# Kernel tuning notes

Measured on AMD Instinct MI355X. Metric: run time of the kernel, lower is better.

The kernel has to match this reference:

```python
import jax, jax.numpy as jnp
import numpy as np
from jax import lax


def setup_inputs() -> dict:
    key = jax.random.key(0)
    k1, k2 = jax.random.split(key)
    B, H, W, Cin, Cout, kh, kw = 16, 128, 128, 128, 128, 3, 3
    X = jax.random.normal(k1, (B, H, W, Cin), dtype=jnp.float32)
    kernel = jax.random.normal(k2, (B, kh, kw, Cin, Cout), dtype=jnp.float32) * 0.05
    return {"X": X, "kernel": kernel}


def _conv_one(x, k):
    # x: [H, W, Cin]; k: [kh, kw, Cin, Cout] -> [H', W', Cout]
    out = lax.conv_general_dilated(
        x[None],  # [1, H, W, Cin]
        k,
        window_strides=(1, 1),
        padding='VALID',
        dimension_numbers=('NHWC', 'HWIO', 'NHWC'),
    )
    return out[0]


def reference(X, kernel):
    # Per-sample dynamic-filter conv: each batch element convolved with its own
    # [kh, kw, Cin, Cout] filter. Equivalent to the TF depthwise-reshape trick
    # followed by reduce_sum over the input-channel axis.
    return jax.vmap(_conv_one)(X, kernel)  # [B, H', W', Cout]
```

## Files before the change

kernel.cpp:

```cpp
#include <hip/hip_runtime.h>
#include <cstdint>

#define OWD 126
#define MTOT 15876

typedef short bf16x8 __attribute__((ext_vector_type(8)));
typedef float f32x4  __attribute__((ext_vector_type(4)));

#define BT_ELEMS  (16u * 128u * 1152u)
#define XBF_ELEMS (16u * 128u * 128u * 128u)
#define WS_NEEDED ((size_t)(BT_ELEMS + XBF_ELEMS) * 2)

__device__ __forceinline__ uint16_t f2bf(float f) {
    union { float f; uint32_t u; } v;
    v.f = f;
    uint32_t u = v.u;
    return (uint16_t)((u + 0x7FFFu + ((u >> 16) & 1u)) >> 16);
}

__device__ __forceinline__ uint32_t pk2(float a, float b) {
    return (uint32_t)f2bf(a) | ((uint32_t)f2bf(b) << 16);
}

__device__ __forceinline__ void gl_lds16(const uint16_t* g, uint16_t* l) {
    __builtin_amdgcn_global_load_lds(
        (const __attribute__((address_space(1))) uint32_t*)g,
        (__attribute__((address_space(3))) uint32_t*)l, 16, 0, 0);
}

__global__ __launch_bounds__(256) void kprep(const float* __restrict__ Kin,
                                             uint16_t* __restrict__ Bt) {
    const int rs = blockIdx.x;
    const int b  = blockIdx.y;
    const int t  = threadIdx.x;
    const int n  = t & 127;
    const int og = t >> 7;

    const float* src = Kin + (((size_t)b * 9 + rs) << 14);
    uint16_t*    dst = Bt + ((size_t)b * 128 + n) * 1152 + rs * 128;

#pragma unroll
    for (int o = 0; o < 8; ++o) {
        const int oct = og * 8 + o;
        const float* s0 = src + (oct * 8) * 128 + n;
        uint4 p;
        p.x = pk2(s0[0 * 128], s0[1 * 128]);
        p.y = pk2(s0[2 * 128], s0[3 * 128]);
        p.z = pk2(s0[4 * 128], s0[5 * 128]);
        p.w = pk2(s0[6 * 128], s0[7 * 128]);
        *(uint4*)(dst + oct * 8) = p;
    }
}

__global__ __launch_bounds__(256) void xprep(const float* __restrict__ X,
                                             uint16_t* __restrict__ Xbf) {
    const size_t i = ((size_t)blockIdx.x * 256 + threadIdx.x) * 8;
    const float4 a = *(const float4*)(X + i);
    const float4 b = *(const float4*)(X + i + 4);
    uint4 p;
    p.x = pk2(a.x, a.y);
    p.y = pk2(a.z, a.w);
    p.z = pk2(b.x, b.y);
    p.w = pk2(b.z, b.w);
    *(uint4*)(Xbf + i) = p;
}

__global__ __launch_bounds__(256) void conv_mfma_a(const uint16_t* __restrict__ Xbf,
                                                   const uint16_t* __restrict__ Bt,
                                                   float* __restrict__ Out) {
    __shared__ __align__(16) uint16_t lA[128 * 32];
    __shared__ __align__(16) uint16_t lB[128 * 32];

    const int mtile = blockIdx.x;
    const int b     = blockIdx.y;
    const int tid   = threadIdx.x;
    const int lane  = tid & 63;
    const int wave  = tid >> 6;
    const int wm    = (wave & 1) << 6;
    const int wn    = (wave >> 1) << 6;
    const int l15   = lane & 15;
    const int quad  = lane >> 4;

    const int row = tid >> 2;
    const int kq  = tid & 3;

    int m0 = mtile * 128 + row;        if (m0 >= MTOT) m0 = MTOT - 1;
    int m1 = mtile * 128 + 64 + row;   if (m1 >= MTOT) m1 = MTOT - 1;
    const int oh0 = m0 / OWD, ow0 = m0 - oh0 * OWD;
    const int oh1 = m1 / OWD, ow1 = m1 - oh1 * OWD;

    const uint16_t* Xr0 = Xbf + (((size_t)b * 128 + oh0) * 128 + ow0) * 128 + kq * 8;
    const uint16_t* Xr1 = Xbf + (((size_t)b * 128 + oh1) * 128 + ow1) * 128 + kq * 8;
    const uint16_t* Br0 = Bt + ((size_t)b * 128 + row) * 1152 + kq * 8;
    const uint16_t* Br1 = Bt + ((size_t)b * 128 + 64 + row) * 1152 + kq * 8;

    uint16_t* lA0 = &lA[tid * 8];
    uint16_t* lA1 = &lA[2048 + tid * 8];
    uint16_t* lB0 = &lB[tid * 8];
    uint16_t* lB1 = &lB[2048 + tid * 8];

    f32x4 acc[4][4];
#pragma unroll
    for (int i = 0; i < 4; ++i)
#pragma unroll
        for (int j = 0; j < 4; ++j)
            acc[i][j] = (f32x4){0.f, 0.f, 0.f, 0.f};

    for (int rs = 0; rs < 9; ++rs) {
        const int r = rs / 3;
        const int s = rs - r * 3;
        const int aoff0 = (r * 128 + s) * 128;
        const int boff0 = rs * 128;
#pragma unroll
        for (int cs = 0; cs < 4; ++cs) {
            const int c0 = cs * 32;

            __syncthreads();
            gl_lds16(Xr0 + aoff0 + c0, lA0);
            gl_lds16(Xr1 + aoff0 + c0, lA1);
            gl_lds16(Br0 + boff0 + c0, lB0);
            gl_lds16(Br1 + boff0 + c0, lB1);
            __syncthreads();

            bf16x8 af[4], bfr[4];
#pragma unroll
            for (int i = 0; i < 4; ++i)
                af[i] = *(const bf16x8*)&lA[(wm + i * 16 + l15) * 32 + quad * 8];
#pragma unroll
            for (int j = 0; j < 4; ++j)
                bfr[j] = *(const bf16x8*)&lB[(wn + j * 16 + l15) * 32 + quad * 8];
#pragma unroll
            for (int i = 0; i < 4; ++i)
#pragma unroll
                for (int j = 0; j < 4; ++j)
                    acc[i][j] = __builtin_amdgcn_mfma_f32_16x16x32_bf16(
                        af[i], bfr[j], acc[i][j], 0, 0, 0);
        }
    }

#pragma unroll
    for (int i = 0; i < 4; ++i) {
#pragma unroll
        for (int rr = 0; rr < 4; ++rr) {
            const int mrow = mtile * 128 + wm + i * 16 + quad * 4 + rr;
            if (mrow < MTOT) {
                const int oh2 = mrow / OWD;
                const int ow2 = mrow - oh2 * OWD;
                float* op = Out + (((size_t)b * OWD + oh2) * OWD + ow2) * 128 + wn + l15;
#pragma unroll
                for (int j = 0; j < 4; ++j)
                    op[j * 16] = acc[i][j][rr];
            }
        }
    }
}

__global__ __launch_bounds__(256) void conv_mfma(const float* __restrict__ X,
                                                 const uint16_t* __restrict__ Bt,
                                                 float* __restrict__ Out) {
    __shared__ __align__(16) uint16_t lA[128 * 64];
    __shared__ __align__(16) uint16_t lB[128 * 64];

    const int mtile = blockIdx.x;
    const int b     = blockIdx.y;
    const int tid   = threadIdx.x;
    const int lane  = tid & 63;
    const int wave  = tid >> 6;
    const int wm    = (wave & 1) << 6;
    const int wn    = (wave >> 1) << 6;
    const int l15   = lane & 15;
    const int quad  = lane >> 4;

    const int srow  = tid >> 1;
    const int shalf = tid & 1;

    int m = mtile * 128 + srow;
    if (m >= MTOT) m = MTOT - 1;
    const int oh = m / OWD;
    const int ow = m - oh * OWD;
    const float*    Xb = X + (((size_t)b * 128 + oh) * 128 + ow) * 128;
    const uint16_t* Bb = Bt + ((size_t)b * 128 + srow) * 1152 + shalf * 32;

    f32x4 acc[4][4];
#pragma unroll
    for (int i = 0; i < 4; ++i)
#pragma unroll
        for (int j = 0; j < 4; ++j)
            acc[i][j] = (f32x4){0.f, 0.f, 0.f, 0.f};

    for (int chunk = 0; chunk < 18; ++chunk) {
        const int rs = chunk >> 1;
        const int c0 = (chunk & 1) << 6;
        const int r  = rs / 3;
        const int s  = rs - r * 3;

        __syncthreads();
        {
            const float4* src = (const float4*)(Xb + (r * 128 + s) * 128 + c0 + shalf * 32);
            float4 v[8];
#pragma unroll
            for (int i = 0; i < 8; ++i) v[i] = src[i];
#pragma unroll
            for (int i = 0; i < 4; ++i) {
                uint4 p;
                p.x = pk2(v[2 * i].x, v[2 * i].y);
                p.y = pk2(v[2 * i].z, v[2 * i].w);
                p.z = pk2(v[2 * i + 1].x, v[2 * i + 1].y);
                p.w = pk2(v[2 * i + 1].z, v[2 * i + 1].w);
                const int ci = (shalf * 4 + i) ^ (srow & 7);
                *(uint4*)&lA[srow * 64 + ci * 8] = p;
            }
        }
        {
            const uint4* bsrc = (const uint4*)(Bb + rs * 128 + c0);
#pragma unroll
            for (int i = 0; i < 4; ++i) {
                const uint4 p = bsrc[i];
                const int ci = (shalf * 4 + i) ^ (srow & 7);
                *(uint4*)&lB[srow * 64 + ci * 8] = p;
            }
        }
        __syncthreads();

#pragma unroll
        for (int ksub = 0; ksub < 2; ++ksub) {
            bf16x8 af[4], bfr[4];
#pragma unroll
            for (int i = 0; i < 4; ++i) {
                const int row = wm + i * 16 + l15;
                const int ci  = (ksub * 4 + quad) ^ (row & 7);
                af[i] = *(const bf16x8*)&lA[row * 64 + ci * 8];
            }
#pragma unroll
            for (int j = 0; j < 4; ++j) {
                const int row = wn + j * 16 + l15;
                const int ci  = (ksub * 4 + quad) ^ (row & 7);
                bfr[j] = *(const bf16x8*)&lB[row * 64 + ci * 8];
            }
#pragma unroll
            for (int i = 0; i < 4; ++i)
#pragma unroll
                for (int j = 0; j < 4; ++j)
                    acc[i][j] = __builtin_amdgcn_mfma_f32_16x16x32_bf16(
                        af[i], bfr[j], acc[i][j], 0, 0, 0);
        }
    }

#pragma unroll
    for (int i = 0; i < 4; ++i) {
#pragma unroll
        for (int rr = 0; rr < 4; ++rr) {
            const int mrow = mtile * 128 + wm + i * 16 + quad * 4 + rr;
            if (mrow < MTOT) {
                const int oh2 = mrow / OWD;
                const int ow2 = mrow - oh2 * OWD;
                float* op = Out + (((size_t)b * OWD + oh2) * OWD + ow2) * 128 + wn + l15;
#pragma unroll
                for (int j = 0; j < 4; ++j)
                    op[j * 16] = acc[i][j][rr];
            }
        }
    }
}

extern "C" void kernel_launch(void* const* d_in, const int* in_sizes, int n_in,
                              void* d_out, int out_size, void* d_ws, size_t ws_size,
                              hipStream_t stream) {
    const float* X   = (const float*)d_in[0];
    const float* Kin = (const float*)d_in[1];
    float*       Out = (float*)d_out;
    uint16_t*    Bt  = (uint16_t*)d_ws;
    uint16_t*    Xbf = Bt + BT_ELEMS;

    kprep<<<dim3(9, 16), 256, 0, stream>>>(Kin, Bt);
    if (ws_size >= WS_NEEDED) {
        xprep<<<XBF_ELEMS / (256 * 8), 256, 0, stream>>>(X, Xbf);
        conv_mfma_a<<<dim3(125, 16), 256, 0, stream>>>(Xbf, Bt, Out);
    } else {
        conv_mfma<<<dim3(125, 16), 256, 0, stream>>>(X, Bt, Out);
    }
}
```

Measured before the change: 345.0 us.

## Double K-chunk per barrier and XOR-swizzle LDS layout to avoid bank conflicts

Each LDS stage now loads a 64-wide K slice instead of 32, which halves the number of syncthreads pairs per tile and runs two MFMA sub-steps per stage. The LDS rows are stored with an XOR swizzle of the 16-byte chunk index by row, and reads apply the same swizzle, so fragment reads spread across banks. The cost is doubled shared memory per block, which may reduce occupancy, plus more address arithmetic.

Measured after the change: 326.7 us. 5.3% less time.

```diff
diff --git a/kernel.cpp b/kernel.cpp
--- a/kernel.cpp
+++ b/kernel.cpp
@@ -68,8 +68,8 @@
 __global__ __launch_bounds__(256) void conv_mfma_a(const uint16_t* __restrict__ Xbf,
                                                    const uint16_t* __restrict__ Bt,
                                                    float* __restrict__ Out) {
-    __shared__ __align__(16) uint16_t lA[128 * 32];
-    __shared__ __align__(16) uint16_t lB[128 * 32];
+    __shared__ __align__(16) uint16_t lA[128 * 64];
+    __shared__ __align__(16) uint16_t lB[128 * 64];
 
     const int mtile = blockIdx.x;
     const int b     = blockIdx.y;
@@ -81,23 +81,20 @@
     const int l15   = lane & 15;
     const int quad  = lane >> 4;
 
-    const int row = tid >> 2;
-    const int kq  = tid & 3;
-
-    int m0 = mtile * 128 + row;        if (m0 >= MTOT) m0 = MTOT - 1;
-    int m1 = mtile * 128 + 64 + row;   if (m1 >= MTOT) m1 = MTOT - 1;
-    const int oh0 = m0 / OWD, ow0 = m0 - oh0 * OWD;
-    const int oh1 = m1 / OWD, ow1 = m1 - oh1 * OWD;
-
-    const uint16_t* Xr0 = Xbf + (((size_t)b * 128 + oh0) * 128 + ow0) * 128 + kq * 8;
-    const uint16_t* Xr1 = Xbf + (((size_t)b * 128 + oh1) * 128 + ow1) * 128 + kq * 8;
-    const uint16_t* Br0 = Bt + ((size_t)b * 128 + row) * 1152 + kq * 8;
-    const uint16_t* Br1 = Bt + ((size_t)b * 128 + 64 + row) * 1152 + kq * 8;
-
-    uint16_t* lA0 = &lA[tid * 8];
-    uint16_t* lA1 = &lA[2048 + tid * 8];
-    uint16_t* lB0 = &lB[tid * 8];
-    uint16_t* lB1 = &lB[2048 + tid * 8];
+    const int kc = (lane & 7) ^ (lane >> 3);
+    const uint16_t* Asrc[4];
+    const uint16_t* Bsrc[4];
+#pragma unroll
+    for (int i = 0; i < 4; ++i) {
+        const int row = wave * 32 + i * 8 + (lane >> 3);
+        int m = mtile * 128 + row;
+        if (m >= MTOT) m = MTOT - 1;
+        const int oh = m / OWD, ow = m - oh * OWD;
+        Asrc[i] = Xbf + (((size_t)b * 128 + oh) * 128 + ow) * 128 + kc * 8;
+        Bsrc[i] = Bt + ((size_t)b * 128 + row) * 1152 + kc * 8;
+    }
+    uint16_t* Adst = &lA[(wave * 256 + lane) * 8];
+    uint16_t* Bdst = &lB[(wave * 256 + lane) * 8];
 
     f32x4 acc[4][4];
 #pragma unroll
@@ -109,32 +106,42 @@
     for (int rs = 0; rs < 9; ++rs) {
         const int r = rs / 3;
         const int s = rs - r * 3;
-        const int aoff0 = (r * 128 + s) * 128;
-        const int boff0 = rs * 128;
-#pragma unroll
-        for (int cs = 0; cs < 4; ++cs) {
-            const int c0 = cs * 32;
+        const int aoff = (r * 128 + s) * 128;
+        const int boff = rs * 128;
+#pragma unroll
+        for (int half = 0; half < 2; ++half) {
+            const int c0 = half * 64;
 
             __syncthreads();
-            gl_lds16(Xr0 + aoff0 + c0, lA0);
-            gl_lds16(Xr1 + aoff0 + c0, lA1);
-            gl_lds16(Br0 + boff0 + c0, lB0);
-            gl_lds16(Br1 + boff0 + c0, lB1);
+#pragma unroll
+            for (int i = 0; i < 4; ++i) {
+                gl_lds16(Asrc[i] + aoff + c0, Adst + i * 512);
+                gl_lds16(Bsrc[i] + boff + c0, Bdst + i * 512);
+            }
             __syncthreads();
 
-            bf16x8 af[4], bfr[4];
-#pragma unroll
-            for (int i = 0; i < 4; ++i)
-                af[i] = *(const bf16x8*)&lA[(wm + i * 16 + l15) * 32 + quad * 8];
-#pragma unroll
-            for (int j = 0; j < 4; ++j)
-                bfr[j] = *(const bf16x8*)&lB[(wn + j * 16 + l15) * 32 + quad * 8];
-#pragma unroll
-            for (int i = 0; i < 4; ++i)
-#pragma unroll
-                for (int j = 0; j < 4; ++j)
-                    acc[i][j] = __builtin_amdgcn_mfma_f32_16x16x32_bf16(
-                        af[i], bfr[j], acc[i][j], 0, 0, 0);
+#pragma unroll
+            for (int ksub = 0; ksub < 2; ++ksub) {
+                bf16x8 af[4], bfr[4];
+#pragma unroll
+                for (int i = 0; i < 4; ++i) {
+                    const int row = wm + i * 16 + l15;
+                    const int pc  = (ksub * 4 + quad) ^ (row & 7);
+                    af[i] = *(const bf16x8*)&lA[row * 64 + pc * 8];
+                }
+#pragma unroll
+                for (int j = 0; j < 4; ++j) {
+                    const int row = wn + j * 16 + l15;
+                    const int pc  = (ksub * 4 + quad) ^ (row & 7);
+                    bfr[j] = *(const bf16x8*)&lB[row * 64 + pc * 8];
+                }
+#pragma unroll
+                for (int i = 0; i < 4; ++i)
+#pragma unroll
+                    for (int j = 0; j < 4; ++j)
+                        acc[i][j] = __builtin_amdgcn_mfma_f32_16x16x32_bf16(
+                            af[i], bfr[j], acc[i][j], 0, 0, 0);
+            }
         }
     }
 
```

## Load MFMA fragments directly from global memory with register double buffering

Applied to the files above, without the earlier changes.

Replaces the LDS-staged tile loads (global_load_lds plus two barriers per K step) with direct per-lane global loads of bf16x8 fragments into registers. A two-buffer register pipeline issues the loads for the next K slice before the MFMAs on the current one, so there is no shared memory and no __syncthreads. This gives up LDS-based reuse across waves, since each wave now fetches its own A and B fragments and relies on L1/L2 to absorb the duplication, and it raises register pressure.

After: 519.5 us. 50.6% more time.

```diff
diff --git a/kernel.cpp b/kernel.cpp
--- a/kernel.cpp
+++ b/kernel.cpp
@@ -20,12 +20,6 @@
 
 __device__ __forceinline__ uint32_t pk2(float a, float b) {
     return (uint32_t)f2bf(a) | ((uint32_t)f2bf(b) << 16);
-}
-
-__device__ __forceinline__ void gl_lds16(const uint16_t* g, uint16_t* l) {
-    __builtin_amdgcn_global_load_lds(
-        (const __attribute__((address_space(1))) uint32_t*)g,
-        (__attribute__((address_space(3))) uint32_t*)l, 16, 0, 0);
 }
 
 __global__ __launch_bounds__(256) void kprep(const float* __restrict__ Kin,
@@ -65,12 +59,9 @@
     *(uint4*)(Xbf + i) = p;
 }
 
-__global__ __launch_bounds__(256) void conv_mfma_a(const uint16_t* __restrict__ Xbf,
+__global__ __launch_bounds__(256) void conv_mfma_b(const uint16_t* __restrict__ Xbf,
                                                    const uint16_t* __restrict__ Bt,
                                                    float* __restrict__ Out) {
-    __shared__ __align__(16) uint16_t lA[128 * 32];
-    __shared__ __align__(16) uint16_t lB[128 * 32];
-
     const int mtile = blockIdx.x;
     const int b     = blockIdx.y;
     const int tid   = threadIdx.x;
@@ -81,23 +72,20 @@
     const int l15   = lane & 15;
     const int quad  = lane >> 4;
 
-    const int row = tid >> 2;
-    const int kq  = tid & 3;
-
-    int m0 = mtile * 128 + row;        if (m0 >= MTOT) m0 = MTOT - 1;
-    int m1 = mtile * 128 + 64 + row;   if (m1 >= MTOT) m1 = MTOT - 1;
-    const int oh0 = m0 / OWD, ow0 = m0 - oh0 * OWD;
-    const int oh1 = m1 / OWD, ow1 = m1 - oh1 * OWD;
-
-    const uint16_t* Xr0 = Xbf + (((size_t)b * 128 + oh0) * 128 + ow0) * 128 + kq * 8;
-    const uint16_t* Xr1 = Xbf + (((size_t)b * 128 + oh1) * 128 + ow1) * 128 + kq * 8;
-    const uint16_t* Br0 = Bt + ((size_t)b * 128 + row) * 1152 + kq * 8;
-    const uint16_t* Br1 = Bt + ((size_t)b * 128 + 64 + row) * 1152 + kq * 8;
-
-    uint16_t* lA0 = &lA[tid * 8];
-    uint16_t* lA1 = &lA[2048 + tid * 8];
-    uint16_t* lB0 = &lB[tid * 8];
-    uint16_t* lB1 = &lB[2048 + tid * 8];
+    const uint16_t* Ap[4];
+#pragma unroll
+    for (int i = 0; i < 4; ++i) {
+        int m = mtile * 128 + wm + i * 16 + l15;
+        if (m >= MTOT) m = MTOT - 1;
+        const int oh = m / OWD, ow = m - oh * OWD;
+        Ap[i] = Xbf + (((size_t)b * 128 + oh) * 128 + ow) * 128 + quad * 8;
+    }
+    const uint16_t* Bp[4];
+#pragma unroll
+    for (int j = 0; j < 4; ++j) {
+        const int n = wn + j * 16 + l15;
+        Bp[j] = Bt + ((size_t)b * 128 + n) * 1152 + quad * 8;
+    }
 
     f32x4 acc[4][4];
 #pragma unroll
@@ -106,37 +94,42 @@
         for (int j = 0; j < 4; ++j)
             acc[i][j] = (f32x4){0.f, 0.f, 0.f, 0.f};
 
-    for (int rs = 0; rs < 9; ++rs) {
-        const int r = rs / 3;
-        const int s = rs - r * 3;
-        const int aoff0 = (r * 128 + s) * 128;
-        const int boff0 = rs * 128;
-#pragma unroll
-        for (int cs = 0; cs < 4; ++cs) {
-            const int c0 = cs * 32;
-
-            __syncthreads();
-            gl_lds16(Xr0 + aoff0 + c0, lA0);
-            gl_lds16(Xr1 + aoff0 + c0, lA1);
-            gl_lds16(Br0 + boff0 + c0, lB0);
-            gl_lds16(Br1 + boff0 + c0, lB1);
-            __syncthreads();
-
-            bf16x8 af[4], bfr[4];
-#pragma unroll
-            for (int i = 0; i < 4; ++i)
-                af[i] = *(const bf16x8*)&lA[(wm + i * 16 + l15) * 32 + quad * 8];
-#pragma unroll
-            for (int j = 0; j < 4; ++j)
-                bfr[j] = *(const bf16x8*)&lB[(wn + j * 16 + l15) * 32 + quad * 8];
-#pragma unroll
-            for (int i = 0; i < 4; ++i)
-#pragma unroll
-                for (int j = 0; j < 4; ++j)
-                    acc[i][j] = __builtin_amdgcn_mfma_f32_16x16x32_bf16(
-                        af[i], bfr[j], acc[i][j], 0, 0, 0);
-        }
-    }
+#define LOADS(s, AF, BF)                                                      \
+    do {                                                                      \
+        const int rs_ = (s) >> 2;                                             \
+        const int r_  = rs_ / 3;                                              \
+        const int sc_ = rs_ - r_ * 3;                                         \
+        const int ao_ = (r_ * 128 + sc_) * 128 + ((s) & 3) * 32;              \
+        const int bo_ = (s) * 32;                                             \
+        _Pragma("unroll") for (int i_ = 0; i_ < 4; ++i_)                      \
+            AF[i_] = *(const bf16x8*)(Ap[i_] + ao_);                          \
+        _Pragma("unroll") for (int j_ = 0; j_ < 4; ++j_)                      \
+            BF[j_] = *(const bf16x8*)(Bp[j_] + bo_);                          \
+    } while (0)
+
+#define MF(AF, BF)                                                            \
+    do {                                                                      \
+        _Pragma("unroll") for (int i_ = 0; i_ < 4; ++i_)                      \
+        _Pragma("unroll") for (int j_ = 0; j_ < 4; ++j_)                      \
+            acc[i_][j_] = __builtin_amdgcn_mfma_f32_16x16x32_bf16(            \
+                AF[i_], BF[j_], acc[i_][j_], 0, 0, 0);                        \
+    } while (0)
+
+    bf16x8 A0[4], B0[4], A1[4], B1[4];
+    LOADS(0, A0, B0);
+#pragma unroll
+    for (int sp = 0; sp < 17; ++sp) {
+        LOADS(2 * sp + 1, A1, B1);
+        MF(A0, B0);
+        LOADS(2 * sp + 2, A0, B0);
+        MF(A1, B1);
+    }
+    LOADS(35, A1, B1);
+    MF(A0, B0);
+    MF(A1, B1);
+
+#undef LOADS
+#undef MF
 
 #pragma unroll
     for (int i = 0; i < 4; ++i) {
@@ -275,7 +268,7 @@
     kprep<<<dim3(9, 16), 256, 0, stream>>>(Kin, Bt);
     if (ws_size >= WS_NEEDED) {
         xprep<<<XBF_ELEMS / (256 * 8), 256, 0, stream>>>(X, Xbf);
-        conv_mfma_a<<<dim3(125, 16), 256, 0, stream>>>(Xbf, Bt, Out);
+        conv_mfma_b<<<dim3(125, 16), 256, 0, stream>>>(Xbf, Bt, Out);
     } else {
         conv_mfma<<<dim3(125, 16), 256, 0, stream>>>(X, Bt, Out);
     }
```
